# Kernel optimization log

Measured on AMD Instinct MI355X. Metric: run time of the kernel, lower is better.

Reference implementation:

```python
import jax, jax.numpy as jnp
import numpy as np

N = 16000      # nodes
E = 256000     # edges
IN0, IN1 = 16, 8   # input irreps: 16x0e + 8x1e  (dim 40)
K0, K1 = 8, 4      # key/query irreps: 8x0e + 4x1e (dim 20)
O0, O1 = 16, 8     # output irreps: 16x0e + 8x1e (dim 40)
NB = 10            # number_of_basis
KWN = IN0*K0 + IN1*K0 + IN0*K1 + IN1*K1 + IN1*K1   # 320 tp weights (key)
VWN = IN0*O0 + IN1*O0 + IN0*O1 + IN1*O1 + IN1*O1   # 640 tp weights (value)
NUM_GROUP = K0 + K1  # len(irreps_key.ls) = 12

# Levi-Civita tensor for the 1e x 1e -> 1e (cross product) path
_EPS = np.zeros((3, 3, 3), dtype=np.float32)
_EPS[0,1,2] = _EPS[1,2,0] = _EPS[2,0,1] = 1.0
_EPS[0,2,1] = _EPS[2,1,0] = _EPS[1,0,2] = -1.0
EPS = jnp.asarray(_EPS)


def _linear_equiv(x, W0, W1, m0, m1):
    # block-diagonal per-irrep linear (o3.Linear, element path normalization)
    x0 = x[:, :m0]                              # [N, m0] scalars
    x1 = x[:, m0:].reshape(x.shape[0], m1, 3)   # [N, m1, 3] vectors
    o0 = (x0 @ W0) / jnp.sqrt(jnp.float32(m0))
    o1 = jnp.einsum('nim,io->nom', x1, W1) / jnp.sqrt(jnp.float32(m1))
    return jnp.concatenate([o0, o1.reshape(x.shape[0], -1)], axis=-1)


def _fc(x, W1, W2):
    # FullyConnectedNet([NB, 16, weight_numel], silu), variance-scaled, no bias
    h = jax.nn.silu((x @ W1) / jnp.sqrt(jnp.float32(NB)))
    return (h @ W2) / jnp.sqrt(jnp.float32(16))


def _tensor_product(x, sh, w, m0, m1, o0, o1):
    # FullyConnectedTensorProduct((m0x0e+m1x1e) x (1x0e+1x1e) -> (o0x0e+o1x1e))
    # with external per-edge weights w [E, weight_numel].
    Ee = x.shape[0]
    x0 = x[:, :m0]                           # [E, m0]
    x1 = x[:, m0:].reshape(Ee, m1, 3)        # [E, m1, 3]
    sh0 = sh[:, :1]                          # [E, 1]
    sh1 = sh[:, 1:4]                         # [E, 3]
    sizes = [m0*o0, m1*o0, m0*o1, m1*o1, m1*o1]
    offs = np.cumsum([0] + sizes)
    w000 = w[:, offs[0]:offs[1]].reshape(Ee, m0, o0)
    w110 = w[:, offs[1]:offs[2]].reshape(Ee, m1, o0)
    w011 = w[:, offs[2]:offs[3]].reshape(Ee, m0, o1)
    w101 = w[:, offs[3]:offs[4]].reshape(Ee, m1, o1)
    w111 = w[:, offs[4]:offs[5]].reshape(Ee, m1, o1)
    s = lambda v: jnp.sqrt(jnp.float32(v))
    # paths into 0e: (0e,0e)->0e and (1e,1e)->0e (dot, CG 1/sqrt(3))
    out0 = (jnp.einsum('ei,eio->eo', x0 * sh0, w000) / s(m0)
            + jnp.einsum('eim,em,eio->eo', x1, sh1, w110) / (s(3) * s(m1))) / s(2)
    # paths into 1e: (0e,1e)->1e, (1e,0e)->1e, (1e,1e)->1e (cross, CG 1/sqrt(2))
    out1 = (jnp.einsum('ei,em,eio->eom', x0, sh1, w011) / s(m0)
            + jnp.einsum('eim,eio->eom', x1 * sh0[:, :, None], w101) / s(m1)
            + jnp.einsum('mab,eia,eb,eio->eom', EPS, x1, sh1, w111) / (s(2) * s(m1))) / s(3)
    return jnp.concatenate([out0, out1.reshape(Ee, o1 * 3)], axis=-1)


def setup_inputs() -> dict:
    key = jax.random.key(0)
    ks = jax.random.split(key, 12)
    feature = jax.random.normal(ks[0], (N, IN0 + IN1 * 3), dtype=jnp.float32)
    edge_src = jax.random.randint(ks[1], (E,), 0, N)
    edge_dst = jax.random.randint(ks[2], (E,), 0, N)
    # spherical harmonics of random edge directions (component norm, lmax=1)
    vec = jax.random.normal(ks[3], (E, 3), dtype=jnp.float32)
    r = jnp.linalg.norm(vec, axis=-1, keepdims=True) + 1e-9
    edge_sh = jnp.concatenate([jnp.ones((E, 1), jnp.float32), jnp.sqrt(3.0) * vec / r], axis=-1)
    # gaussian radial basis of edge lengths
    centers = jnp.linspace(0.0, 2.0, NB)
    edge_length_embedded = jnp.exp(-((r - centers[None, :]) ** 2) / 0.08).astype(jnp.float32)
    Wq0 = jax.random.normal(ks[4], (IN0, K0), dtype=jnp.float32)
    Wq1 = jax.random.normal(ks[5], (IN1, K1), dtype=jnp.float32)
    Wk1 = jax.random.normal(ks[6], (NB, 16), dtype=jnp.float32)
    Wk2 = jax.random.normal(ks[7], (16, KWN), dtype=jnp.float32)
    Wv1 = jax.random.normal(ks[8], (NB, 16), dtype=jnp.float32)
    Wv2 = jax.random.normal(ks[9], (16, VWN), dtype=jnp.float32)
    return {"feature": feature, "edge_src": edge_src, "edge_dst": edge_dst,
            "edge_sh": edge_sh, "edge_length_embedded": edge_length_embedded,
            "Wq0": Wq0, "Wq1": Wq1, "Wk1": Wk1, "Wk2": Wk2, "Wv1": Wv1, "Wv2": Wv2}


def reference(feature, edge_src, edge_dst, edge_sh, edge_length_embedded,
              Wq0, Wq1, Wk1, Wk2, Wv1, Wv2):
    # query: per-node equivariant linear
    q = _linear_equiv(feature, Wq0, Wq1, IN0, IN1)           # [N, 20]
    xd = feature[edge_dst]                                    # [E, 40]
    # key / value: per-edge tensor product with radially-generated weights
    k = _tensor_product(xd, edge_sh, _fc(edge_length_embedded, Wk1, Wk2), IN0, IN1, K0, K1)  # [E, 20]
    v = _tensor_product(xd, edge_sh, _fc(edge_length_embedded, Wv1, Wv2), IN0, IN1, O0, O1)  # [E, 40]
    logit = jnp.sum(q[edge_src] * k, axis=-1) / jnp.sqrt(jnp.float32(NUM_GROUP))  # [E]
    # scatter_logsumexp over edge_src
    m = jax.ops.segment_max(logit, edge_src, num_segments=N)
    z = jax.ops.segment_sum(jnp.exp(logit - m[edge_src]), edge_src, num_segments=N)
    log_Z = m + jnp.log(z)
    alpha = jnp.exp(logit - log_Z[edge_src])                  # [E]
    out = jax.ops.segment_sum(alpha[:, None] * v, edge_src, num_segments=N)  # [N, 40]
    return out
```

## Files before the change

### kernel.cpp

```cpp
#include <hip/hip_runtime.h>
#include <math.h>

#define NN 16000
#define NE 256000


__device__ __forceinline__ float wdot(const float* __restrict__ wt, const float* h) {
    float w = 0.f;
#pragma unroll
    for (int c = 0; c < 16; ++c) w = fmaf(h[c], wt[c], w);
    return w;
}

__device__ __forceinline__ float segsum(float v, unsigned addmask) {
#pragma unroll
    for (int k = 0, off = 1; off < 64; ++k, off <<= 1) {
        float ov = __shfl_down(v, off);
        if (addmask & (1u << k)) v += ov;
    }
    return v;
}

#define C_000 0.17677669529663687f
#define C_110 0.14433756729740643f
#define C_011 0.14433756729740643f
#define C_101 0.20412414523193148f
#define RS10  0.31622776601683794f
#define RS12  0.28867513459481287f

__global__ void prep_kernel(const float* __restrict__ Wk2, const float* __restrict__ Wv2,
                            float* __restrict__ Wk2t, float* __restrict__ Wv2t) {
    int tid = blockIdx.x * blockDim.x + threadIdx.x;
    if (tid < 320 * 16) {
        int j = tid >> 4, c = tid & 15;
        Wk2t[tid] = 0.25f * Wk2[c * 320 + j];
    }
    int t2 = tid - 320 * 16;
    if (t2 >= 0 && t2 < 640 * 16) {
        int j = t2 >> 4, c = t2 & 15;
        Wv2t[t2] = 0.25f * Wv2[c * 640 + j];
    }
}

__global__ void q_kernel(const float* __restrict__ feature,
                         const float* __restrict__ Wq0, const float* __restrict__ Wq1,
                         float* __restrict__ qbuf) {
    int n = blockIdx.x * blockDim.x + threadIdx.x;
    if (n >= NN) return;
    const float4* f4 = (const float4*)(feature + n * 40);
    float xr[40];
#pragma unroll
    for (int i = 0; i < 10; ++i) {
        float4 t = f4[i];
        xr[i * 4 + 0] = t.x; xr[i * 4 + 1] = t.y; xr[i * 4 + 2] = t.z; xr[i * 4 + 3] = t.w;
    }
    float* qr = qbuf + n * 20;
#pragma unroll 1
    for (int o = 0; o < 8; ++o) {
        float a = 0.f;
#pragma unroll
        for (int i = 0; i < 16; ++i) a = fmaf(xr[i], Wq0[i * 8 + o], a);
        qr[o] = 0.25f * a;
    }
#pragma unroll 1
    for (int o = 0; o < 4; ++o) {
        float a0 = 0.f, a1 = 0.f, a2 = 0.f;
#pragma unroll
        for (int i = 0; i < 8; ++i) {
            float w = Wq1[i * 4 + o];
            a0 = fmaf(xr[16 + i * 3 + 0], w, a0);
            a1 = fmaf(xr[16 + i * 3 + 1], w, a1);
            a2 = fmaf(xr[16 + i * 3 + 2], w, a2);
        }
        qr[8 + o * 3 + 0] = 0.35355339059327373f * a0;
        qr[8 + o * 3 + 1] = 0.35355339059327373f * a1;
        qr[8 + o * 3 + 2] = 0.35355339059327373f * a2;
    }
}

__global__ void hist_kernel(const int* __restrict__ esrc, int* __restrict__ cnt) {
    int e = blockIdx.x * blockDim.x + threadIdx.x;
    if (e < NE) atomicAdd(cnt + esrc[e], 1);
}

__global__ void scan_kernel(const int* __restrict__ cnt,
                            int* __restrict__ rowstart, int* __restrict__ cursor) {
    __shared__ int part[1024];
    int t = threadIdx.x;
    int base = t * 16;
    int local[16];
    int s = 0;
#pragma unroll
    for (int j = 0; j < 16; ++j) {
        int idx = base + j;
        int c = (idx < NN) ? cnt[idx] : 0;
        local[j] = s;
        s += c;
    }
    part[t] = s;
    __syncthreads();
    for (int off = 1; off < 1024; off <<= 1) {
        int v = (t >= off) ? part[t - off] : 0;
        __syncthreads();
        part[t] += v;
        __syncthreads();
    }
    int excl = part[t] - s;
#pragma unroll
    for (int j = 0; j < 16; ++j) {
        int idx = base + j;
        if (idx < NN) {
            int val = excl + local[j];
            rowstart[idx] = val;
            cursor[idx] = val;
        } else if (idx == NN) {
            rowstart[NN] = excl + local[j];
        }
    }
}

__global__ void scatter_kernel(const int* __restrict__ esrc, const int* __restrict__ edst,
                               int* __restrict__ cursor, int* __restrict__ perm,
                               int* __restrict__ srcS, int* __restrict__ dstS) {
    int e = blockIdx.x * blockDim.x + threadIdx.x;
    if (e >= NE) return;
    int src = esrc[e];
    int pos = atomicAdd(cursor + src, 1);
    perm[pos] = e;
    srcS[pos] = src;
    dstS[pos] = edst[e];
}

__global__ __launch_bounds__(256)
void k_kernel(const int* __restrict__ perm, const int* __restrict__ srcS,
              const int* __restrict__ dstS,
              const float* __restrict__ esh, const float* __restrict__ elen,
              const float* __restrict__ feature, const float* __restrict__ qbuf,
              const float* __restrict__ Wk1, const float* __restrict__ Wk2t,
              float* __restrict__ logitbuf) {
    int sidx = blockIdx.x * blockDim.x + threadIdx.x;
    if (sidx >= NE) return;
    int e = perm[sidx], src = srcS[sidx], dst = dstS[sidx];

    float4 shv = *(const float4*)(esh + e * 4);
    float sh0 = shv.x, sh1x = shv.y, sh1y = shv.z, sh1z = shv.w;

    const float* el = elen + e * 10;
    float h[16];
    {
        float acc[16];
#pragma unroll
        for (int j = 0; j < 16; ++j) acc[j] = 0.f;
#pragma unroll
        for (int c = 0; c < 10; ++c) {
            float ec = el[c];
#pragma unroll
            for (int j = 0; j < 16; ++j) acc[j] = fmaf(ec, Wk1[c * 16 + j], acc[j]);
        }
#pragma unroll
        for (int j = 0; j < 16; ++j) {
            float s = acc[j] * RS10;
            h[j] = s / (1.f + expf(-s));
        }
    }

    const float4* f4 = (const float4*)(feature + dst * 40);
    float xr[40];
#pragma unroll
    for (int i = 0; i < 10; ++i) {
        float4 t = f4[i];
        xr[i * 4 + 0] = t.x; xr[i * 4 + 1] = t.y; xr[i * 4 + 2] = t.z; xr[i * 4 + 3] = t.w;
    }
    float x0[16];
#pragma unroll
    for (int i = 0; i < 16; ++i) x0[i] = xr[i];
    float x1[8][3], d1[8], cx[8][3];
#pragma unroll
    for (int i = 0; i < 8; ++i) {
        float a = xr[16 + i * 3 + 0], b = xr[16 + i * 3 + 1], c = xr[16 + i * 3 + 2];
        x1[i][0] = a; x1[i][1] = b; x1[i][2] = c;
        d1[i] = a * sh1x + b * sh1y + c * sh1z;
        cx[i][0] = b * sh1z - c * sh1y;
        cx[i][1] = c * sh1x - a * sh1z;
        cx[i][2] = a * sh1y - b * sh1x;
    }

    const float* qr = qbuf + src * 20;
    float logit = 0.f;

#pragma unroll 1
    for (int o = 0; o < 8; ++o) {
        float e000 = 0.f, e110 = 0.f;
#pragma unroll
        for (int i = 0; i < 16; ++i)
            e000 = fmaf(x0[i], wdot(Wk2t + (i * 8 + o) * 16, h), e000);
#pragma unroll
        for (int i = 0; i < 8; ++i)
            e110 = fmaf(d1[i], wdot(Wk2t + ((128 + i * 8 + o)) * 16, h), e110);
        float ko = fmaf(C_000 * sh0, e000, C_110 * e110);
        logit = fmaf(qr[o], ko, logit);
    }
#pragma unroll 1
    for (int o = 0; o < 4; ++o) {
        float c0 = 0.f;
#pragma unroll
        for (int i = 0; i < 16; ++i)
            c0 = fmaf(x0[i], wdot(Wk2t + ((192 + i * 4 + o)) * 16, h), c0);
        float s1x = 0.f, s1y = 0.f, s1z = 0.f, s2x = 0.f, s2y = 0.f, s2z = 0.f;
#pragma unroll
        for (int i = 0; i < 8; ++i) {
            float wa = wdot(Wk2t + ((256 + i * 4 + o)) * 16, h);
            float wb = wdot(Wk2t + ((288 + i * 4 + o)) * 16, h);
            s1x = fmaf(x1[i][0], wa, s1x); s1y = fmaf(x1[i][1], wa, s1y); s1z = fmaf(x1[i][2], wa, s1z);
            s2x = fmaf(cx[i][0], wb, s2x); s2y = fmaf(cx[i][1], wb, s2y); s2z = fmaf(cx[i][2], wb, s2z);
        }
        float kx = C_011 * fmaf(c0, sh1x, s2x) + C_101 * sh0 * s1x;
        float ky = C_011 * fmaf(c0, sh1y, s2y) + C_101 * sh0 * s1y;
        float kz = C_011 * fmaf(c0, sh1z, s2z) + C_101 * sh0 * s1z;
        logit = fmaf(qr[8 + o * 3 + 0], kx, logit);
        logit = fmaf(qr[8 + o * 3 + 1], ky, logit);
        logit = fmaf(qr[8 + o * 3 + 2], kz, logit);
    }

    logitbuf[sidx] = logit * RS12;
}

__global__ void mz_kernel(const int* __restrict__ rowstart,
                          const float* __restrict__ logitbuf, float* __restrict__ logZ) {
    int n = blockIdx.x * blockDim.x + threadIdx.x;
    if (n >= NN) return;
    int b = rowstart[n], e2 = rowstart[n + 1];
    if (b >= e2) { logZ[n] = 0.f; return; }
    float m = -INFINITY;
    for (int i = b; i < e2; ++i) m = fmaxf(m, logitbuf[i]);
    float z = 0.f;
    for (int i = b; i < e2; ++i) z += expf(logitbuf[i] - m);
    logZ[n] = m + logf(z);
}

__global__ __launch_bounds__(256)
void v_kernel(const int* __restrict__ perm, const int* __restrict__ srcS,
              const int* __restrict__ dstS,
              const float* __restrict__ esh, const float* __restrict__ elen,
              const float* __restrict__ feature,
              const float* __restrict__ logitbuf, const float* __restrict__ logZ,
              const float* __restrict__ Wv1, const float* __restrict__ Wv2t,
              float* __restrict__ out) {
    int sidx = blockIdx.x * blockDim.x + threadIdx.x;
    if (sidx >= NE) return;
    int e = perm[sidx], src = srcS[sidx], dst = dstS[sidx];
    int lane = threadIdx.x & 63;

    int srcPrev = __shfl_up(src, 1);
    bool head = (lane == 0) || (srcPrev != src);
    unsigned addmask = 0;
#pragma unroll
    for (int k = 0, off = 1; off < 64; ++k, off <<= 1) {
        int os = __shfl_down(src, off);
        if ((lane + off) < 64 && os == src) addmask |= (1u << k);
    }

    float alpha = expf(logitbuf[sidx] - logZ[src]);

    float4 shv = *(const float4*)(esh + e * 4);
    float sh0 = shv.x, sh1x = shv.y, sh1y = shv.z, sh1z = shv.w;

    const float* el = elen + e * 10;
    float h[16];
    {
        float acc[16];
#pragma unroll
        for (int j = 0; j < 16; ++j) acc[j] = 0.f;
#pragma unroll
        for (int c = 0; c < 10; ++c) {
            float ec = el[c];
#pragma unroll
            for (int j = 0; j < 16; ++j) acc[j] = fmaf(ec, Wv1[c * 16 + j], acc[j]);
        }
#pragma unroll
        for (int j = 0; j < 16; ++j) {
            float s = acc[j] * RS10;
            h[j] = s / (1.f + expf(-s));
        }
    }

    const float4* f4 = (const float4*)(feature + dst * 40);
    float xr[40];
#pragma unroll
    for (int i = 0; i < 10; ++i) {
        float4 t = f4[i];
        xr[i * 4 + 0] = t.x; xr[i * 4 + 1] = t.y; xr[i * 4 + 2] = t.z; xr[i * 4 + 3] = t.w;
    }
    float x0[16];
#pragma unroll
    for (int i = 0; i < 16; ++i) x0[i] = xr[i];
    float x1[8][3], d1[8], cx[8][3];
#pragma unroll
    for (int i = 0; i < 8; ++i) {
        float a = xr[16 + i * 3 + 0], b = xr[16 + i * 3 + 1], c = xr[16 + i * 3 + 2];
        x1[i][0] = a; x1[i][1] = b; x1[i][2] = c;
        d1[i] = a * sh1x + b * sh1y + c * sh1z;
        cx[i][0] = b * sh1z - c * sh1y;
        cx[i][1] = c * sh1x - a * sh1z;
        cx[i][2] = a * sh1y - b * sh1x;
    }

    float* orow = out + src * 40;

#pragma unroll 1
    for (int o = 0; o < 16; ++o) {
        float e000 = 0.f, e110 = 0.f;
#pragma unroll
        for (int i = 0; i < 16; ++i)
            e000 = fmaf(x0[i], wdot(Wv2t + (i * 16 + o) * 16, h), e000);
#pragma unroll
        for (int i = 0; i < 8; ++i)
            e110 = fmaf(d1[i], wdot(Wv2t + ((256 + i * 16 + o)) * 16, h), e110);
        float vo = alpha * fmaf(C_000 * sh0, e000, C_110 * e110);
        vo = segsum(vo, addmask);
        if (head) atomicAdd(orow + o, vo);
    }
#pragma unroll 1
    for (int o = 0; o < 8; ++o) {
        float c0 = 0.f;
#pragma unroll
        for (int i = 0; i < 16; ++i)
            c0 = fmaf(x0[i], wdot(Wv2t + ((384 + i * 8 + o)) * 16, h), c0);
        float s1x = 0.f, s1y = 0.f, s1z = 0.f, s2x = 0.f, s2y = 0.f, s2z = 0.f;
#pragma unroll
        for (int i = 0; i < 8; ++i) {
            float wa = wdot(Wv2t + ((512 + i * 8 + o)) * 16, h);
            float wb = wdot(Wv2t + ((576 + i * 8 + o)) * 16, h);
            s1x = fmaf(x1[i][0], wa, s1x); s1y = fmaf(x1[i][1], wa, s1y); s1z = fmaf(x1[i][2], wa, s1z);
            s2x = fmaf(cx[i][0], wb, s2x); s2y = fmaf(cx[i][1], wb, s2y); s2z = fmaf(cx[i][2], wb, s2z);
        }
        float vx = alpha * (C_011 * fmaf(c0, sh1x, s2x) + C_101 * sh0 * s1x);
        float vy = alpha * (C_011 * fmaf(c0, sh1y, s2y) + C_101 * sh0 * s1y);
        float vz = alpha * (C_011 * fmaf(c0, sh1z, s2z) + C_101 * sh0 * s1z);
        vx = segsum(vx, addmask);
        vy = segsum(vy, addmask);
        vz = segsum(vz, addmask);
        if (head) {
            atomicAdd(orow + 16 + o * 3 + 0, vx);
            atomicAdd(orow + 16 + o * 3 + 1, vy);
            atomicAdd(orow + 16 + o * 3 + 2, vz);
        }
    }
}

extern "C" void kernel_launch(void* const* d_in, const int* in_sizes, int n_in,
                              void* d_out, int out_size, void* d_ws, size_t ws_size,
                              hipStream_t stream) {
    const float* feature = (const float*)d_in[0];
    const int*   esrc    = (const int*)d_in[1];
    const int*   edst    = (const int*)d_in[2];
    const float* esh     = (const float*)d_in[3];
    const float* elen    = (const float*)d_in[4];
    const float* Wq0     = (const float*)d_in[5];
    const float* Wq1     = (const float*)d_in[6];
    const float* Wk1     = (const float*)d_in[7];
    const float* Wk2     = (const float*)d_in[8];
    const float* Wv1     = (const float*)d_in[9];
    const float* Wv2     = (const float*)d_in[10];
    float* out = (float*)d_out;

    float* ws = (float*)d_ws;
    float* qbuf     = ws;
    float* logitbuf = ws + 320000;
    float* logZ     = ws + 576000;
    float* Wk2t     = ws + 592000;
    float* Wv2t     = ws + 597120;
    int*   cnt      = (int*)(ws + 607360);
    int*   rowstart = (int*)(ws + 623360);
    int*   cursor   = (int*)(ws + 639361);
    int*   perm     = (int*)(ws + 655361);
    int*   srcS     = (int*)(ws + 911361);
    int*   dstS     = (int*)(ws + 1167361);

    hipMemsetAsync(cnt, 0, NN * sizeof(int), stream);
    hipMemsetAsync(out, 0, (size_t)out_size * sizeof(float), stream);

    prep_kernel<<<60, 256, 0, stream>>>(Wk2, Wv2, Wk2t, Wv2t);
    q_kernel<<<(NN + 255) / 256, 256, 0, stream>>>(feature, Wq0, Wq1, qbuf);
    hist_kernel<<<NE / 256, 256, 0, stream>>>(esrc, cnt);
    scan_kernel<<<1, 1024, 0, stream>>>(cnt, rowstart, cursor);
    scatter_kernel<<<NE / 256, 256, 0, stream>>>(esrc, edst, cursor, perm, srcS, dstS);
    k_kernel<<<NE / 256, 256, 0, stream>>>(perm, srcS, dstS, esh, elen, feature, qbuf,
                                           Wk1, Wk2t, logitbuf);
    mz_kernel<<<(NN + 255) / 256, 256, 0, stream>>>(rowstart, logitbuf, logZ);
    v_kernel<<<NE / 256, 256, 0, stream>>>(perm, srcS, dstS, esh, elen, feature,
                                           logitbuf, logZ, Wv1, Wv2t, out);
}
```

Measured before the change: 400.4 us.

## Pre-permute edge SH and radial embeddings into sorted order, batch segmented shuffles

The scatter kernel now writes edge_sh and edge_length_embedded into src-sorted buffers, so the k and v kernels read them contiguously by sorted index instead of gathering through a perm array. The v kernel also groups four scalar outputs (and three vector components) per shuffle-reduction pass, interleaving independent shuffles before the atomics. This costs an extra write of sorted copies in the scatter kernel and more live registers in the v kernel.

After: 411.4 us. +2.7%, slower.

```diff
diff --git a/kernel.cpp b/kernel.cpp
--- a/kernel.cpp
+++ b/kernel.cpp
@@ -10,15 +10,6 @@
 #pragma unroll
     for (int c = 0; c < 16; ++c) w = fmaf(h[c], wt[c], w);
     return w;
-}
-
-__device__ __forceinline__ float segsum(float v, unsigned addmask) {
-#pragma unroll
-    for (int k = 0, off = 1; off < 64; ++k, off <<= 1) {
-        float ov = __shfl_down(v, off);
-        if (addmask & (1u << k)) v += ov;
-    }
-    return v;
 }
 
 #define C_000 0.17677669529663687f
@@ -120,32 +111,42 @@
 }
 
 __global__ void scatter_kernel(const int* __restrict__ esrc, const int* __restrict__ edst,
-                               int* __restrict__ cursor, int* __restrict__ perm,
-                               int* __restrict__ srcS, int* __restrict__ dstS) {
+                               const float* __restrict__ esh, const float* __restrict__ elen,
+                               int* __restrict__ cursor,
+                               int* __restrict__ srcS, int* __restrict__ dstS,
+                               float* __restrict__ shS, float* __restrict__ elenS) {
     int e = blockIdx.x * blockDim.x + threadIdx.x;
     if (e >= NE) return;
     int src = esrc[e];
     int pos = atomicAdd(cursor + src, 1);
-    perm[pos] = e;
     srcS[pos] = src;
     dstS[pos] = edst[e];
+    *(float4*)(shS + pos * 4) = *(const float4*)(esh + e * 4);
+    const float2* ep = (const float2*)(elen + e * 10);
+    float2* op = (float2*)(elenS + pos * 10);
+#pragma unroll
+    for (int j = 0; j < 5; ++j) op[j] = ep[j];
 }
 
 __global__ __launch_bounds__(256)
-void k_kernel(const int* __restrict__ perm, const int* __restrict__ srcS,
-              const int* __restrict__ dstS,
-              const float* __restrict__ esh, const float* __restrict__ elen,
+void k_kernel(const int* __restrict__ srcS, const int* __restrict__ dstS,
+              const float* __restrict__ shS, const float* __restrict__ elenS,
               const float* __restrict__ feature, const float* __restrict__ qbuf,
               const float* __restrict__ Wk1, const float* __restrict__ Wk2t,
               float* __restrict__ logitbuf) {
     int sidx = blockIdx.x * blockDim.x + threadIdx.x;
     if (sidx >= NE) return;
-    int e = perm[sidx], src = srcS[sidx], dst = dstS[sidx];
-
-    float4 shv = *(const float4*)(esh + e * 4);
+    int src = srcS[sidx], dst = dstS[sidx];
+
+    float4 shv = *(const float4*)(shS + sidx * 4);
     float sh0 = shv.x, sh1x = shv.y, sh1y = shv.z, sh1z = shv.w;
 
-    const float* el = elen + e * 10;
+    float el[10];
+    {
+        const float2* ep = (const float2*)(elenS + sidx * 10);
+#pragma unroll
+        for (int j = 0; j < 5; ++j) { float2 t = ep[j]; el[j * 2] = t.x; el[j * 2 + 1] = t.y; }
+    }
     float h[16];
     {
         float acc[16];
@@ -239,16 +240,15 @@
 }
 
 __global__ __launch_bounds__(256)
-void v_kernel(const int* __restrict__ perm, const int* __restrict__ srcS,
-              const int* __restrict__ dstS,
-              const float* __restrict__ esh, const float* __restrict__ elen,
+void v_kernel(const int* __restrict__ srcS, const int* __restrict__ dstS,
+              const float* __restrict__ shS, const float* __restrict__ elenS,
               const float* __restrict__ feature,
               const float* __restrict__ logitbuf, const float* __restrict__ logZ,
               const float* __restrict__ Wv1, const float* __restrict__ Wv2t,
               float* __restrict__ out) {
     int sidx = blockIdx.x * blockDim.x + threadIdx.x;
     if (sidx >= NE) return;
-    int e = perm[sidx], src = srcS[sidx], dst = dstS[sidx];
+    int src = srcS[sidx], dst = dstS[sidx];
     int lane = threadIdx.x & 63;
 
     int srcPrev = __shfl_up(src, 1);
@@ -262,10 +262,15 @@
 
     float alpha = expf(logitbuf[sidx] - logZ[src]);
 
-    float4 shv = *(const float4*)(esh + e * 4);
+    float4 shv = *(const float4*)(shS + sidx * 4);
     float sh0 = shv.x, sh1x = shv.y, sh1y = shv.z, sh1z = shv.w;
 
-    const float* el = elen + e * 10;
+    float el[10];
+    {
+        const float2* ep = (const float2*)(elenS + sidx * 10);
+#pragma unroll
+        for (int j = 0; j < 5; ++j) { float2 t = ep[j]; el[j * 2] = t.x; el[j * 2 + 1] = t.y; }
+    }
     float h[16];
     {
         float acc[16];
@@ -308,18 +313,37 @@
     float* orow = out + src * 40;
 
 #pragma unroll 1
-    for (int o = 0; o < 16; ++o) {
-        float e000 = 0.f, e110 = 0.f;
-#pragma unroll
-        for (int i = 0; i < 16; ++i)
-            e000 = fmaf(x0[i], wdot(Wv2t + (i * 16 + o) * 16, h), e000);
-#pragma unroll
-        for (int i = 0; i < 8; ++i)
-            e110 = fmaf(d1[i], wdot(Wv2t + ((256 + i * 16 + o)) * 16, h), e110);
-        float vo = alpha * fmaf(C_000 * sh0, e000, C_110 * e110);
-        vo = segsum(vo, addmask);
-        if (head) atomicAdd(orow + o, vo);
-    }
+    for (int og = 0; og < 4; ++og) {
+        int obase = og * 4;
+        float grp[4];
+#pragma unroll
+        for (int oo = 0; oo < 4; ++oo) {
+            int o = obase + oo;
+            float e000 = 0.f, e110 = 0.f;
+#pragma unroll
+            for (int i = 0; i < 16; ++i)
+                e000 = fmaf(x0[i], wdot(Wv2t + (i * 16 + o) * 16, h), e000);
+#pragma unroll
+            for (int i = 0; i < 8; ++i)
+                e110 = fmaf(d1[i], wdot(Wv2t + ((256 + i * 16 + o)) * 16, h), e110);
+            grp[oo] = alpha * fmaf(C_000 * sh0, e000, C_110 * e110);
+        }
+#pragma unroll
+        for (int k2 = 0, off = 1; off < 64; ++k2, off <<= 1) {
+            float t0 = __shfl_down(grp[0], off);
+            float t1 = __shfl_down(grp[1], off);
+            float t2 = __shfl_down(grp[2], off);
+            float t3 = __shfl_down(grp[3], off);
+            if (addmask & (1u << k2)) { grp[0] += t0; grp[1] += t1; grp[2] += t2; grp[3] += t3; }
+        }
+        if (head) {
+            atomicAdd(orow + obase + 0, grp[0]);
+            atomicAdd(orow + obase + 1, grp[1]);
+            atomicAdd(orow + obase + 2, grp[2]);
+            atomicAdd(orow + obase + 3, grp[3]);
+        }
+    }
+
 #pragma unroll 1
     for (int o = 0; o < 8; ++o) {
         float c0 = 0.f;
@@ -337,9 +361,13 @@
         float vx = alpha * (C_011 * fmaf(c0, sh1x, s2x) + C_101 * sh0 * s1x);
         float vy = alpha * (C_011 * fmaf(c0, sh1y, s2y) + C_101 * sh0 * s1y);
         float vz = alpha * (C_011 * fmaf(c0, sh1z, s2z) + C_101 * sh0 * s1z);
-        vx = segsum(vx, addmask);
-        vy = segsum(vy, addmask);
-        vz = segsum(vz, addmask);
+#pragma unroll
+        for (int k2 = 0, off = 1; off < 64; ++k2, off <<= 1) {
+            float t0 = __shfl_down(vx, off);
+            float t1 = __shfl_down(vy, off);
+            float t2 = __shfl_down(vz, off);
+            if (addmask & (1u << k2)) { vx += t0; vy += t1; vz += t2; }
+        }
         if (head) {
             atomicAdd(orow + 16 + o * 3 + 0, vx);
             atomicAdd(orow + 16 + o * 3 + 1, vy);
@@ -373,9 +401,13 @@
     int*   cnt      = (int*)(ws + 607360);
     int*   rowstart = (int*)(ws + 623360);
     int*   cursor   = (int*)(ws + 639361);
-    int*   perm     = (int*)(ws + 655361);
-    int*   srcS     = (int*)(ws + 911361);
-    int*   dstS     = (int*)(ws + 1167361);
+    int*   srcS     = (int*)(ws + 655361);
+    int*   dstS     = (int*)(ws + 911361);
+    float* shS      = ws + 1167361;
+    float* elenS    = ws + 2191361;
+
+    shS   = ws + 1167364;
+    elenS = ws + 2191364;
 
     hipMemsetAsync(cnt, 0, NN * sizeof(int), stream);
     hipMemsetAsync(out, 0, (size_t)out_size * sizeof(float), stream);
@@ -384,10 +416,11 @@
     q_kernel<<<(NN + 255) / 256, 256, 0, stream>>>(feature, Wq0, Wq1, qbuf);
     hist_kernel<<<NE / 256, 256, 0, stream>>>(esrc, cnt);
     scan_kernel<<<1, 1024, 0, stream>>>(cnt, rowstart, cursor);
-    scatter_kernel<<<NE / 256, 256, 0, stream>>>(esrc, edst, cursor, perm, srcS, dstS);
-    k_kernel<<<NE / 256, 256, 0, stream>>>(perm, srcS, dstS, esh, elen, feature, qbuf,
+    scatter_kernel<<<NE / 256, 256, 0, stream>>>(esrc, edst, esh, elen, cursor,
+                                                 srcS, dstS, shS, elenS);
+    k_kernel<<<NE / 256, 256, 0, stream>>>(srcS, dstS, shS, elenS, feature, qbuf,
                                            Wk1, Wk2t, logitbuf);
     mz_kernel<<<(NN + 255) / 256, 256, 0, stream>>>(rowstart, logitbuf, logZ);
-    v_kernel<<<NE / 256, 256, 0, stream>>>(perm, srcS, dstS, esh, elen, feature,
+    v_kernel<<<NE / 256, 256, 0, stream>>>(srcS, dstS, shS, elenS, feature,
                                            logitbuf, logZ, Wv1, Wv2t, out);
 }
```
